# Optimization experiments

Measured on AMD Instinct MI355X. Metric: run time of the kernel, lower is better.

## Reference

```python
import jax, jax.numpy as jnp
import numpy as np

B, S, H, HEADS, STEP = 128, 256, 128, 8, 1


def setup_inputs() -> dict:
    key = jax.random.key(0)
    ks = jax.random.split(key, 20)
    rn = lambda k, shape: jax.random.normal(k, shape, dtype=jnp.float32) * 0.1
    return {
        "A": jax.random.uniform(ks[0], (B, S, 2 * S), dtype=jnp.float32),
        "hidden": jax.random.normal(ks[1], (B, S, H), dtype=jnp.float32),
        "mask": jnp.ones((B, S), dtype=jnp.int32),
        "w_ih": rn(ks[2], (3 * H, 2 * H)),
        "w_hh": rn(ks[3], (3 * H, H)),
        "b_ih": rn(ks[4], (3 * H,)),
        "b_hh": rn(ks[5], (3 * H,)),
        "b_iah": rn(ks[6], (H,)),
        "b_oah": rn(ks[7], (H,)),
        "W_ein": rn(ks[8], (H, H)), "b_ein": rn(ks[9], (H,)),
        "W_eout": rn(ks[10], (H, H)), "b_eout": rn(ks[11], (H,)),
        "W_q0": rn(ks[12], (H, H)), "b_q0": rn(ks[13], (H,)),
        "W_q1": rn(ks[14], (H, H)), "b_q1": rn(ks[15], (H,)),
        "W_q2": rn(ks[16], (H, H)), "b_q2": rn(ks[17], (H,)),
    }


def _forward(A, hidden, mask, w_ih, w_hh, b_ih, b_hh, b_iah, b_oah,
             W_ein, b_ein, W_eout, b_eout, W_q0, b_q0, W_q1, b_q1, W_q2, b_q2):
    b, s, h = hidden.shape
    dk = h // HEADS
    # ---- GNN: gated graph propagation (GRU cell over adjacency messages) ----
    for _ in range(STEP):
        msg_in = A[:, :, :s] @ (hidden @ W_ein.T + b_ein) + b_iah    # [B,S,H]
        msg_out = A[:, :, s:] @ (hidden @ W_eout.T + b_eout) + b_oah  # [B,S,H]
        inputs = jnp.concatenate([msg_in, msg_out], axis=2)           # [B,S,2H]
        gi = inputs @ w_ih.T + b_ih                                   # [B,S,3H]
        gh = hidden @ w_hh.T + b_hh                                   # [B,S,3H]
        i_r, i_i, i_n = jnp.split(gi, 3, axis=2)
        h_r, h_i, h_n = jnp.split(gh, 3, axis=2)
        resetgate = jax.nn.sigmoid(i_r + h_r)
        inputgate = jax.nn.sigmoid(i_i + h_i)
        newgate = jnp.tanh(i_n + resetgate * h_n)
        hidden = hidden - inputgate * (hidden - newgate)
    # ---- query: hidden state of the last valid item in each session ----
    last_idx = jnp.sum(mask, axis=1) - 1
    ht1 = hidden[jnp.arange(b), last_idx]                             # [B,H]
    # ---- LastAttenion: sigmoid score + double softmax readout ----
    q0 = (ht1 @ W_q0.T + b_q0).reshape(b, HEADS, dk)                  # [B,h,dk]
    q1 = (hidden @ W_q1.T + b_q1).reshape(b, s, HEADS, dk).transpose(0, 2, 1, 3)
    q2 = (hidden @ W_q2.T + b_q2).reshape(b, s, HEADS, dk).transpose(0, 2, 1, 3)
    # q0 is expanded over the query axis, so every score row is identical
    alpha = jax.nn.sigmoid(jnp.einsum('bhd,bhjd->bhj', q0, q1))        # [B,h,S]
    alpha = jnp.broadcast_to(alpha[:, :, None, :], (b, HEADS, s, s))   # [B,h,S,S]
    alpha = jax.nn.softmax(alpha, axis=-1)
    row_keep = (mask > 0)[:, None, :, None]                            # [B,1,S,1]
    alpha = jnp.where(row_keep, alpha, -jnp.inf)
    alpha = jax.nn.softmax(2.0 * alpha, axis=1)                        # over heads
    alpha = jnp.where(row_keep, alpha, 0.0)  # guard fully-masked rows (torch would NaN)
    x = jnp.einsum('bhij,bhjd->bhid', alpha, q2)                       # [B,h,S,dk]
    x = x.transpose(0, 2, 1, 3).reshape(b, s, h)                       # [B,S,H]
    a = jnp.sum(x * mask[:, :, None].astype(x.dtype), axis=1)          # [B,H]
    return a


def reference(A, hidden, mask, w_ih, w_hh, b_ih, b_hh, b_iah, b_oah,
              W_ein, b_ein, W_eout, b_eout, W_q0, b_q0, W_q1, b_q1, W_q2, b_q2):
    return _forward(A, hidden, mask, w_ih, w_hh, b_ih, b_hh, b_iah, b_oah,
                    W_ein, b_ein, W_eout, b_eout, W_q0, b_q0, W_q1, b_q1, W_q2, b_q2)
```

## Files before the change

### kernel.cpp

```cpp
#include <hip/hip_runtime.h>
#include <cstdint>
#include <cstddef>

#define BB   128
#define SS   256
#define HH   128
#define NH   8
#define DKK  16

typedef unsigned short u16;
typedef __attribute__((ext_vector_type(8))) short   sh8;
typedef __attribute__((ext_vector_type(4))) float   f32x4;

__device__ __forceinline__ float sigmoidf_(float x) { return 1.f / (1.f + expf(-x)); }

__device__ __forceinline__ u16 f2bf(float x) {
    union { float f; unsigned int u; } v; v.f = x;
    unsigned int r = (v.u + 0x7fffu + ((v.u >> 16) & 1u)) >> 16;
    return (u16)r;
}
__device__ __forceinline__ float bf2f(u16 u) {
    union { unsigned int u; float f; } v; v.u = ((unsigned int)u) << 16;
    return v.f;
}

#define BKk 32
#define PK  40

template<int XMODE, int OMODE>
__global__ __launch_bounds__(256) void gemm_mfma(
    const void* __restrict__ Xa, const void* __restrict__ Xc, int ldx, int ldx1, int ksplit,
    long long sXb, long long sXh,
    const u16* __restrict__ Bw, int ldb, long long sBb, long long sBh,
    const float* __restrict__ bias,
    void* __restrict__ Out, long long ldo, long long sOb, long long sOh,
    int K)
{
    __shared__ u16 As[128 * PK];
    __shared__ u16 Bs[128 * PK];

    const int t  = threadIdx.x;
    const int bm = blockIdx.x * 128;
    const int bn = blockIdx.y * 128;
    const long long zb = blockIdx.z >> 1, zh = blockIdx.z & 1;

    const u16* Bp = Bw + zb * sBb + zh * sBh;

    const int wave = t >> 6, lane = t & 63;
    const int wr = (wave >> 1) * 64, wc = (wave & 1) * 64;
    const int fm = lane & 15, fq = lane >> 4;

    f32x4 acc[4][4] = {};

    const int r0  = t >> 2, kk0 = (t & 3) * 8;
    const int r1  = t >> 3, kk1 = (t & 7) * 4;

    for (int k0 = 0; k0 < K; k0 += BKk) {
        if (XMODE == 1) {
            const float* Xf = (const float*)Xa + zb * sXb + zh * sXh;
            #pragma unroll
            for (int c = 0; c < 4; c++) {
                int r = r1 + 32 * c;
                float4 v = *(const float4*)(Xf + (long long)(bm + r) * ldx + k0 + kk1);
                ushort4 w = { f2bf(v.x), f2bf(v.y), f2bf(v.z), f2bf(v.w) };
                *(ushort4*)&As[r * PK + kk1] = w;
            }
        } else {
            #pragma unroll
            for (int c = 0; c < 2; c++) {
                int r = r0 + 64 * c;
                const u16* src;
                if (XMODE == 2 && k0 >= ksplit)
                    src = (const u16*)Xc + (long long)(bm + r) * ldx1 + (k0 - ksplit) + kk0;
                else
                    src = (const u16*)Xa + (long long)(bm + r) * ldx + k0 + kk0;
                uint4 v = *(const uint4*)src;
                *(uint4*)&As[r * PK + kk0] = v;
            }
        }
        #pragma unroll
        for (int c = 0; c < 2; c++) {
            int r = r0 + 64 * c;
            uint4 v = *(const uint4*)(Bp + (long long)(bn + r) * ldb + k0 + kk0);
            *(uint4*)&Bs[r * PK + kk0] = v;
        }
        __syncthreads();

        sh8 af[4], bfr[4];
        #pragma unroll
        for (int i = 0; i < 4; i++) af[i]  = *(const sh8*)&As[(wr + i * 16 + fm) * PK + fq * 8];
        #pragma unroll
        for (int j = 0; j < 4; j++) bfr[j] = *(const sh8*)&Bs[(wc + j * 16 + fm) * PK + fq * 8];
        #pragma unroll
        for (int i = 0; i < 4; i++)
            #pragma unroll
            for (int j = 0; j < 4; j++)
                acc[i][j] = __builtin_amdgcn_mfma_f32_16x16x32_bf16(af[i], bfr[j], acc[i][j], 0, 0, 0);
        __syncthreads();
    }

    #pragma unroll
    for (int j = 0; j < 4; j++) {
        const int col = bn + wc + j * 16 + fm;
        const float bj = bias ? bias[col] : 0.f;
        #pragma unroll
        for (int i = 0; i < 4; i++) {
            const int row0 = bm + wr + i * 16 + fq * 4;
            if (OMODE == 0) {
                float* O = (float*)Out + zb * sOb + zh * sOh;
                #pragma unroll
                for (int r = 0; r < 4; r++)
                    O[(long long)(row0 + r) * ldo + col] = acc[i][j][r] + bj;
            } else if (OMODE == 1) {
                u16* O = (u16*)Out + zb * sOb + zh * sOh;
                #pragma unroll
                for (int r = 0; r < 4; r++)
                    O[(long long)(row0 + r) * ldo + col] = f2bf(acc[i][j][r] + bj);
            } else {
                u16* O = (u16*)Out + zb * sOb + zh * sOh;
                ushort4 w = { f2bf(acc[i][j][0] + bj), f2bf(acc[i][j][1] + bj),
                              f2bf(acc[i][j][2] + bj), f2bf(acc[i][j][3] + bj) };
                *(ushort4*)&O[(long long)col * ldo + row0] = w;
            }
        }
    }
}

__global__ __launch_bounds__(256) void k_prepw(
    const float* __restrict__ w_ih, const float* __restrict__ w_hh,
    const float* __restrict__ b_ih, const float* __restrict__ b_hh,
    const float* __restrict__ b_iah, const float* __restrict__ b_oah,
    const float* __restrict__ W_ein, const float* __restrict__ b_ein,
    const float* __restrict__ W_eout, const float* __restrict__ b_eout,
    const float* __restrict__ W_q1, const float* __restrict__ b_q1,
    const float* __restrict__ W_q2, const float* __restrict__ b_q2,
    u16* __restrict__ W2bf, float* __restrict__ bias2,
    u16* __restrict__ Wcat, float* __restrict__ biascat,
    u16* __restrict__ Wq12, float* __restrict__ biasq12)
{
    int idx = blockIdx.x * 256 + threadIdx.x;
    if (idx < 512 * 384) {
        int n = idx / 384, kk = idx % 384;
        float v;
        if (n < 384) v = (kk < 256) ? w_ih[n * 256 + kk]
                                    : (n < 256 ? w_hh[n * 128 + kk - 256] : 0.f);
        else         v = (kk < 256) ? 0.f : w_hh[(n - 128) * 128 + kk - 256];
        W2bf[idx] = f2bf(v);
    }
    if (idx < 256 * 128) {
        int n = idx >> 7, k = idx & 127;
        Wcat[idx] = f2bf(n < 128 ? W_ein[n * 128 + k] : W_eout[(n - 128) * 128 + k]);
        Wq12[idx] = f2bf(n < 128 ? W_q1[n * 128 + k]  : W_q2[(n - 128) * 128 + k]);
    }
    if (idx < 512) {
        int n = idx;
        float s;
        if (n < 256)      s = b_ih[n] + b_hh[n];
        else if (n < 384) s = b_ih[n];
        else              s = b_hh[n - 128];
        if (n < 384) {
            for (int k = 0; k < 128; k++)
                s += w_ih[n * 256 + k] * b_iah[k] + w_ih[n * 256 + 128 + k] * b_oah[k];
        }
        bias2[n] = s;
    }
    if (idx < 256) {
        biascat[idx] = idx < 128 ? b_ein[idx] : b_eout[idx - 128];
        biasq12[idx] = idx < 128 ? b_q1[idx]  : b_q2[idx - 128];
    }
}

__global__ __launch_bounds__(256) void k_cast4(const float* __restrict__ in,
                                               u16* __restrict__ outp, int n4)
{
    int i = blockIdx.x * 256 + threadIdx.x;
    if (i < n4) {
        float4 v = ((const float4*)in)[i];
        ushort4 w = { f2bf(v.x), f2bf(v.y), f2bf(v.z), f2bf(v.w) };
        ((ushort4*)outp)[i] = w;
    }
}

__global__ void k_mask(const int* __restrict__ mask, int* __restrict__ lastidx,
                       int* __restrict__ nvalid)
{
    int b = threadIdx.x;
    int s = 0;
    for (int j = 0; j < SS; j++) s += mask[b * SS + j];
    nvalid[b] = s;
    lastidx[b] = (s - 1) & (SS - 1);
}

__global__ __launch_bounds__(256) void k_gates(const float* __restrict__ g4,
                                               const float* __restrict__ hidden,
                                               u16* __restrict__ hnew_bf)
{
    size_t idx = (size_t)blockIdx.x * 256 + threadIdx.x;
    int c = (int)(idx & 127);
    size_t row = idx >> 7;
    const float* g = g4 + row * 512;
    float gr  = g[c];
    float gi  = g[128 + c];
    float in_ = g[256 + c];
    float hn  = g[384 + c];
    float h = hidden[idx];
    float r  = sigmoidf_(gr);
    float ig = sigmoidf_(gi);
    float ng = tanhf(in_ + r * hn);
    hnew_bf[idx] = f2bf(h - ig * (h - ng));
}

__global__ void k_q0(const u16* __restrict__ hnew_bf, const int* __restrict__ lastidx,
                     const float* __restrict__ Wq0, const float* __restrict__ bq0,
                     float* __restrict__ q0buf)
{
    int b = blockIdx.x;
    int n = threadIdx.x;
    __shared__ float hs[HH];
    const u16* hrow = hnew_bf + ((size_t)b * SS + lastidx[b]) * HH;
    hs[n] = bf2f(hrow[n]);
    __syncthreads();
    float s = bq0[n];
    const float* w = Wq0 + (size_t)n * HH;
    #pragma unroll 8
    for (int k = 0; k < HH; k++) s += hs[k] * w[k];
    q0buf[(size_t)b * HH + n] = s;
}

__global__ __launch_bounds__(256) void k_scores(const float* __restrict__ q0buf,
                                                const float* __restrict__ q12,
                                                float* __restrict__ pbuf)
{
    int h = blockIdx.x;
    int b = blockIdx.y;
    int j = threadIdx.x;
    __shared__ float q0s[DKK];
    __shared__ float red[SS];
    if (j < DKK) q0s[j] = q0buf[(size_t)b * HH + h * DKK + j];
    __syncthreads();

    const float4* q1p = (const float4*)(q12 + ((size_t)b * SS + j) * 256 + h * DKK);
    float4 v0 = q1p[0], v1 = q1p[1], v2 = q1p[2], v3 = q1p[3];
    float s = 0.f;
    s += q0s[0] * v0.x + q0s[1] * v0.y + q0s[2] * v0.z + q0s[3] * v0.w;
    s += q0s[4] * v1.x + q0s[5] * v1.y + q0s[6] * v1.z + q0s[7] * v1.w;
    s += q0s[8] * v2.x + q0s[9] * v2.y + q0s[10] * v2.z + q0s[11] * v2.w;
    s += q0s[12] * v3.x + q0s[13] * v3.y + q0s[14] * v3.z + q0s[15] * v3.w;
    float a = sigmoidf_(s);

    red[j] = a;
    __syncthreads();
    for (int off = 128; off > 0; off >>= 1) {
        if (j < off) red[j] = fmaxf(red[j], red[j + off]);
        __syncthreads();
    }
    float m = red[0];
    __syncthreads();
    float e = expf(a - m);
    red[j] = e;
    __syncthreads();
    for (int off = 128; off > 0; off >>= 1) {
        if (j < off) red[j] += red[j + off];
        __syncthreads();
    }
    float denom = red[0];
    pbuf[((size_t)b * NH + h) * SS + j] = e / denom;
}

__global__ __launch_bounds__(128) void k_readout(const float* __restrict__ pbuf,
                                                 const float* __restrict__ q12,
                                                 const int* __restrict__ nvalid,
                                                 float* __restrict__ out)
{
    int b = blockIdx.x;
    int t = threadIdx.x;
    __shared__ float w_s[NH][SS];

    #pragma unroll
    for (int jj = 0; jj < 2; jj++) {
        int j = t + jj * 128;
        float e[NH];
        float den = 0.f;
        #pragma unroll
        for (int h = 0; h < NH; h++) {
            float p = pbuf[((size_t)b * NH + h) * SS + j];
            e[h] = expf(2.f * p);
            den += e[h];
        }
        float inv = 1.f / den;
        #pragma unroll
        for (int h = 0; h < NH; h++) w_s[h][j] = e[h] * inv;
    }
    __syncthreads();

    int h = t >> 4;
    float acc = 0.f;
    const float* q2b = q12 + (size_t)b * SS * 256 + 128 + t;
    for (int j = 0; j < SS; j++) acc += w_s[h][j] * q2b[(size_t)j * 256];
    out[(size_t)b * HH + t] = acc * (float)nvalid[b];
}

extern "C" void kernel_launch(void* const* d_in, const int* in_sizes, int n_in,
                              void* d_out, int out_size, void* d_ws, size_t ws_size,
                              hipStream_t stream)
{
    const float* A      = (const float*)d_in[0];
    const float* hidden = (const float*)d_in[1];
    const int*   mask   = (const int*)d_in[2];
    const float* w_ih   = (const float*)d_in[3];
    const float* w_hh   = (const float*)d_in[4];
    const float* b_ih   = (const float*)d_in[5];
    const float* b_hh   = (const float*)d_in[6];
    const float* b_iah  = (const float*)d_in[7];
    const float* b_oah  = (const float*)d_in[8];
    const float* W_ein  = (const float*)d_in[9];
    const float* b_ein  = (const float*)d_in[10];
    const float* W_eout = (const float*)d_in[11];
    const float* b_eout = (const float*)d_in[12];
    const float* W_q0   = (const float*)d_in[13];
    const float* b_q0   = (const float*)d_in[14];
    const float* W_q1   = (const float*)d_in[15];
    const float* b_q1   = (const float*)d_in[16];
    const float* W_q2   = (const float*)d_in[17];
    const float* b_q2   = (const float*)d_in[18];
    float* out = (float*)d_out;
    char* ws = (char*)d_ws;

    u16*   Et      = (u16*)(ws + 0);
    u16*   Mbuf    = (u16*)(ws + 16777216);
    float* q12     = (float*)(ws + 0);
    u16*   h_bf    = (u16*)(ws + 33554432);
    u16*   hnew_bf = (u16*)(ws + 41943040);
    u16*   W2bf    = (u16*)(ws + 50331648);
    u16*   Wcat    = (u16*)(ws + 50724864);
    u16*   Wq12    = (u16*)(ws + 50790400);
    float* bias2   = (float*)(ws + 50855936);
    float* biascat = (float*)(ws + 50857984);
    float* biasq12 = (float*)(ws + 50859008);
    float* q0buf   = (float*)(ws + 50860032);
    float* pbuf    = (float*)(ws + 50925568);
    int*   lastidx = (int*)(ws + 51974144);
    int*   nvalid  = (int*)(ws + 51974656);
    float* g4 = (float*)d_in[0];

    k_prepw<<<768, 256, 0, stream>>>(w_ih, w_hh, b_ih, b_hh, b_iah, b_oah,
                                     W_ein, b_ein, W_eout, b_eout,
                                     W_q1, b_q1, W_q2, b_q2,
                                     W2bf, bias2, Wcat, biascat, Wq12, biasq12);
    k_mask<<<1, 128, 0, stream>>>(mask, lastidx, nvalid);
    k_cast4<<<4096, 256, 0, stream>>>(hidden, h_bf, 1048576);

    gemm_mfma<0, 2><<<dim3(256, 2, 1), 256, 0, stream>>>(
        h_bf, nullptr, 128, 0, 0, 0, 0,
        Wcat, 128, 0, 0, biascat,
        Et, 32768, 0, 0, 128);

    gemm_mfma<1, 1><<<dim3(2, 1, 256), 256, 0, stream>>>(
        A, nullptr, 512, 0, 0, 131072LL, 256LL,
        Et, 32768, 256LL, 128LL * 32768LL, nullptr,
        Mbuf, 256, 65536LL, 128LL, 256);

    gemm_mfma<2, 0><<<dim3(256, 4, 1), 256, 0, stream>>>(
        Mbuf, h_bf, 256, 128, 256, 0, 0,
        W2bf, 384, 0, 0, bias2,
        g4, 512, 0, 0, 384);

    k_gates<<<16384, 256, 0, stream>>>(g4, hidden, hnew_bf);

    gemm_mfma<0, 0><<<dim3(256, 2, 1), 256, 0, stream>>>(
        hnew_bf, nullptr, 128, 0, 0, 0, 0,
        Wq12, 128, 0, 0, biasq12,
        q12, 256, 0, 0, 128);

    k_q0<<<BB, HH, 0, stream>>>(hnew_bf, lastidx, W_q0, b_q0, q0buf);
    k_scores<<<dim3(NH, BB), SS, 0, stream>>>(q0buf, q12, pbuf);
    k_readout<<<BB, HH, 0, stream>>>(pbuf, q12, nvalid, out);
}
```

Baseline: 258.8 us.

## Fuse GRU gates into GEMM epilogue, fold hidden cast, merge attention tail

Interleaves the GRU weight rows so each group of four output columns holds r/i/n_in/n_h for one channel. The gate math then runs in the GEMM epilogue through lane shuffles, which removes the fp32 g4 round-trip and the separate gates kernel. The hidden→bf16 cast is folded into the GEMM A-load path, q1/q2 are stored as bf16, and the mask/q0/scores/readout kernels are merged into one per-batch tail kernel. This cuts launches and memory traffic. In exchange, the epilogue uses scattered stores with a quarter of the lanes active, and q12 loses precision by going to bf16.

```diff
diff --git a/kernel.cpp b/kernel.cpp
--- a/kernel.cpp
+++ b/kernel.cpp
@@ -34,7 +34,7 @@
     const u16* __restrict__ Bw, int ldb, long long sBb, long long sBh,
     const float* __restrict__ bias,
     void* __restrict__ Out, long long ldo, long long sOb, long long sOh,
-    int K)
+    int K, const float* __restrict__ hid)
 {
     __shared__ u16 As[128 * PK];
     __shared__ u16 Bs[128 * PK];
@@ -56,12 +56,18 @@
     const int r1  = t >> 3, kk1 = (t & 7) * 4;
 
     for (int k0 = 0; k0 < K; k0 += BKk) {
-        if (XMODE == 1) {
-            const float* Xf = (const float*)Xa + zb * sXb + zh * sXh;
+        if (XMODE == 1 || (XMODE == 3 && k0 >= ksplit)) {
+            const float* Xf;
+            int kb, ld;
+            if (XMODE == 1) {
+                Xf = (const float*)Xa + zb * sXb + zh * sXh; kb = k0; ld = ldx;
+            } else {
+                Xf = (const float*)Xc; kb = k0 - ksplit; ld = ldx1;
+            }
             #pragma unroll
             for (int c = 0; c < 4; c++) {
                 int r = r1 + 32 * c;
-                float4 v = *(const float4*)(Xf + (long long)(bm + r) * ldx + k0 + kk1);
+                float4 v = *(const float4*)(Xf + (long long)(bm + r) * ld + kb + kk1);
                 ushort4 w = { f2bf(v.x), f2bf(v.y), f2bf(v.z), f2bf(v.w) };
                 *(ushort4*)&As[r * PK + kk1] = w;
             }
@@ -69,11 +75,7 @@
             #pragma unroll
             for (int c = 0; c < 2; c++) {
                 int r = r0 + 64 * c;
-                const u16* src;
-                if (XMODE == 2 && k0 >= ksplit)
-                    src = (const u16*)Xc + (long long)(bm + r) * ldx1 + (k0 - ksplit) + kk0;
-                else
-                    src = (const u16*)Xa + (long long)(bm + r) * ldx + k0 + kk0;
+                const u16* src = (const u16*)Xa + (long long)(bm + r) * ldx + k0 + kk0;
                 uint4 v = *(const uint4*)src;
                 *(uint4*)&As[r * PK + kk0] = v;
             }
@@ -106,21 +108,35 @@
         #pragma unroll
         for (int i = 0; i < 4; i++) {
             const int row0 = bm + wr + i * 16 + fq * 4;
-            if (OMODE == 0) {
-                float* O = (float*)Out + zb * sOb + zh * sOh;
-                #pragma unroll
-                for (int r = 0; r < 4; r++)
-                    O[(long long)(row0 + r) * ldo + col] = acc[i][j][r] + bj;
-            } else if (OMODE == 1) {
+            if (OMODE == 1) {
                 u16* O = (u16*)Out + zb * sOb + zh * sOh;
                 #pragma unroll
                 for (int r = 0; r < 4; r++)
                     O[(long long)(row0 + r) * ldo + col] = f2bf(acc[i][j][r] + bj);
-            } else {
+            } else if (OMODE == 2) {
                 u16* O = (u16*)Out + zb * sOb + zh * sOh;
                 ushort4 w = { f2bf(acc[i][j][0] + bj), f2bf(acc[i][j][1] + bj),
                               f2bf(acc[i][j][2] + bj), f2bf(acc[i][j][3] + bj) };
                 *(ushort4*)&O[(long long)col * ldo + row0] = w;
+            } else {
+                u16* O = (u16*)Out;
+                const bool act = (fm & 3) == 0;
+                const int ch = ((bn + wc + j * 16) >> 2) + (fm >> 2);
+                #pragma unroll
+                for (int r = 0; r < 4; r++) {
+                    float v  = acc[i][j][r] + bj;
+                    float a1 = __shfl_xor(v, 1);
+                    float a2 = __shfl_xor(v, 2);
+                    float a3 = __shfl_xor(a1, 2);
+                    if (act) {
+                        const int row = row0 + r;
+                        float h  = hid[(long long)row * HH + ch];
+                        float rg = sigmoidf_(v);
+                        float ig = sigmoidf_(a1);
+                        float ng = tanhf(a2 + rg * a3);
+                        O[(long long)row * ldo + ch] = f2bf(h - ig * (h - ng));
+                    }
+                }
             }
         }
     }
@@ -140,11 +156,13 @@
 {
     int idx = blockIdx.x * 256 + threadIdx.x;
     if (idx < 512 * 384) {
-        int n = idx / 384, kk = idx % 384;
+        int np = idx / 384, kk = idx % 384;
+        int c = np >> 2, g = np & 3;
         float v;
-        if (n < 384) v = (kk < 256) ? w_ih[n * 256 + kk]
-                                    : (n < 256 ? w_hh[n * 128 + kk - 256] : 0.f);
-        else         v = (kk < 256) ? 0.f : w_hh[(n - 128) * 128 + kk - 256];
+        if (g < 2)       v = (kk < 256) ? w_ih[(g * 128 + c) * 256 + kk]
+                                        : w_hh[(g * 128 + c) * 128 + kk - 256];
+        else if (g == 2) v = (kk < 256) ? w_ih[(256 + c) * 256 + kk] : 0.f;
+        else             v = (kk < 256) ? 0.f : w_hh[(256 + c) * 128 + kk - 256];
         W2bf[idx] = f2bf(v);
     }
     if (idx < 256 * 128) {
@@ -153,16 +171,17 @@
         Wq12[idx] = f2bf(n < 128 ? W_q1[n * 128 + k]  : W_q2[(n - 128) * 128 + k]);
     }
     if (idx < 512) {
-        int n = idx;
+        int np = idx, c = np >> 2, g = np & 3;
         float s;
-        if (n < 256)      s = b_ih[n] + b_hh[n];
-        else if (n < 384) s = b_ih[n];
-        else              s = b_hh[n - 128];
-        if (n < 384) {
+        if (g < 2)       s = b_ih[g * 128 + c] + b_hh[g * 128 + c];
+        else if (g == 2) s = b_ih[256 + c];
+        else             s = b_hh[256 + c];
+        if (g < 3) {
+            int n = (g < 2) ? g * 128 + c : 256 + c;
             for (int k = 0; k < 128; k++)
                 s += w_ih[n * 256 + k] * b_iah[k] + w_ih[n * 256 + 128 + k] * b_oah[k];
         }
-        bias2[n] = s;
+        bias2[np] = s;
     }
     if (idx < 256) {
         biascat[idx] = idx < 128 ? b_ein[idx] : b_eout[idx - 128];
@@ -170,134 +189,96 @@
     }
 }
 
-__global__ __launch_bounds__(256) void k_cast4(const float* __restrict__ in,
-                                               u16* __restrict__ outp, int n4)
+__global__ __launch_bounds__(256) void k_tail(
+    const u16* __restrict__ hnew_bf, const int* __restrict__ mask,
+    const u16* __restrict__ q12, const float* __restrict__ Wq0,
+    const float* __restrict__ bq0, float* __restrict__ out)
 {
-    int i = blockIdx.x * 256 + threadIdx.x;
-    if (i < n4) {
-        float4 v = ((const float4*)in)[i];
-        ushort4 w = { f2bf(v.x), f2bf(v.y), f2bf(v.z), f2bf(v.w) };
-        ((ushort4*)outp)[i] = w;
-    }
-}
-
-__global__ void k_mask(const int* __restrict__ mask, int* __restrict__ lastidx,
-                       int* __restrict__ nvalid)
-{
-    int b = threadIdx.x;
-    int s = 0;
-    for (int j = 0; j < SS; j++) s += mask[b * SS + j];
-    nvalid[b] = s;
-    lastidx[b] = (s - 1) & (SS - 1);
-}
-
-__global__ __launch_bounds__(256) void k_gates(const float* __restrict__ g4,
-                                               const float* __restrict__ hidden,
-                                               u16* __restrict__ hnew_bf)
-{
-    size_t idx = (size_t)blockIdx.x * 256 + threadIdx.x;
-    int c = (int)(idx & 127);
-    size_t row = idx >> 7;
-    const float* g = g4 + row * 512;
-    float gr  = g[c];
-    float gi  = g[128 + c];
-    float in_ = g[256 + c];
-    float hn  = g[384 + c];
-    float h = hidden[idx];
-    float r  = sigmoidf_(gr);
-    float ig = sigmoidf_(gi);
-    float ng = tanhf(in_ + r * hn);
-    hnew_bf[idx] = f2bf(h - ig * (h - ng));
-}
-
-__global__ void k_q0(const u16* __restrict__ hnew_bf, const int* __restrict__ lastidx,
-                     const float* __restrict__ Wq0, const float* __restrict__ bq0,
-                     float* __restrict__ q0buf)
-{
-    int b = blockIdx.x;
-    int n = threadIdx.x;
+    const int b = blockIdx.x, t = threadIdx.x;
+    __shared__ float red[256];
     __shared__ float hs[HH];
-    const u16* hrow = hnew_bf + ((size_t)b * SS + lastidx[b]) * HH;
-    hs[n] = bf2f(hrow[n]);
-    __syncthreads();
-    float s = bq0[n];
-    const float* w = Wq0 + (size_t)n * HH;
-    #pragma unroll 8
-    for (int k = 0; k < HH; k++) s += hs[k] * w[k];
-    q0buf[(size_t)b * HH + n] = s;
-}
-
-__global__ __launch_bounds__(256) void k_scores(const float* __restrict__ q0buf,
-                                                const float* __restrict__ q12,
-                                                float* __restrict__ pbuf)
-{
-    int h = blockIdx.x;
-    int b = blockIdx.y;
-    int j = threadIdx.x;
-    __shared__ float q0s[DKK];
-    __shared__ float red[SS];
-    if (j < DKK) q0s[j] = q0buf[(size_t)b * HH + h * DKK + j];
-    __syncthreads();
-
-    const float4* q1p = (const float4*)(q12 + ((size_t)b * SS + j) * 256 + h * DKK);
-    float4 v0 = q1p[0], v1 = q1p[1], v2 = q1p[2], v3 = q1p[3];
-    float s = 0.f;
-    s += q0s[0] * v0.x + q0s[1] * v0.y + q0s[2] * v0.z + q0s[3] * v0.w;
-    s += q0s[4] * v1.x + q0s[5] * v1.y + q0s[6] * v1.z + q0s[7] * v1.w;
-    s += q0s[8] * v2.x + q0s[9] * v2.y + q0s[10] * v2.z + q0s[11] * v2.w;
-    s += q0s[12] * v3.x + q0s[13] * v3.y + q0s[14] * v3.z + q0s[15] * v3.w;
-    float a = sigmoidf_(s);
-
-    red[j] = a;
+    __shared__ float q0s[HH];
+    __shared__ float p_s[NH][SS];
+    __shared__ float w_s[NH][SS];
+    __shared__ int s_nv;
+
+    red[t] = (float)mask[b * SS + t];
     __syncthreads();
     for (int off = 128; off > 0; off >>= 1) {
-        if (j < off) red[j] = fmaxf(red[j], red[j + off]);
+        if (t < off) red[t] += red[t + off];
         __syncthreads();
     }
-    float m = red[0];
-    __syncthreads();
-    float e = expf(a - m);
-    red[j] = e;
-    __syncthreads();
-    for (int off = 128; off > 0; off >>= 1) {
-        if (j < off) red[j] += red[j + off];
-        __syncthreads();
-    }
-    float denom = red[0];
-    pbuf[((size_t)b * NH + h) * SS + j] = e / denom;
-}
-
-__global__ __launch_bounds__(128) void k_readout(const float* __restrict__ pbuf,
-                                                 const float* __restrict__ q12,
-                                                 const int* __restrict__ nvalid,
-                                                 float* __restrict__ out)
-{
-    int b = blockIdx.x;
-    int t = threadIdx.x;
-    __shared__ float w_s[NH][SS];
-
-    #pragma unroll
-    for (int jj = 0; jj < 2; jj++) {
-        int j = t + jj * 128;
-        float e[NH];
-        float den = 0.f;
+    if (t == 0) s_nv = (int)red[0];
+    __syncthreads();
+    const int nv = s_nv;
+    const int last = (nv - 1) & (SS - 1);
+
+    if (t < HH) hs[t] = bf2f(hnew_bf[((size_t)b * SS + last) * HH + t]);
+    __syncthreads();
+
+    {
+        const int n = t & 127, kh = t >> 7;
+        const float* w = Wq0 + (size_t)n * HH + kh * 64;
+        float s = 0.f;
+        #pragma unroll 16
+        for (int k = 0; k < 64; k++) s += hs[kh * 64 + k] * w[k];
+        red[t] = s;
+    }
+    __syncthreads();
+    if (t < HH) q0s[t] = red[t] + red[t + 128] + bq0[t];
+    __syncthreads();
+
+    {
+        const u16* q1r = q12 + ((size_t)b * SS + t) * 256;
         #pragma unroll
         for (int h = 0; h < NH; h++) {
-            float p = pbuf[((size_t)b * NH + h) * SS + j];
-            e[h] = expf(2.f * p);
-            den += e[h];
-        }
-        float inv = 1.f / den;
-        #pragma unroll
-        for (int h = 0; h < NH; h++) w_s[h][j] = e[h] * inv;
-    }
-    __syncthreads();
-
-    int h = t >> 4;
-    float acc = 0.f;
-    const float* q2b = q12 + (size_t)b * SS * 256 + 128 + t;
-    for (int j = 0; j < SS; j++) acc += w_s[h][j] * q2b[(size_t)j * 256];
-    out[(size_t)b * HH + t] = acc * (float)nvalid[b];
+            float s = 0.f;
+            #pragma unroll
+            for (int d = 0; d < DKK; d++) s += q0s[h * DKK + d] * bf2f(q1r[h * DKK + d]);
+            p_s[h][t] = sigmoidf_(s);
+        }
+    }
+    __syncthreads();
+
+    {
+        const int h = t >> 5, l = t & 31;
+        float v[8], m = -1e30f;
+        #pragma unroll
+        for (int u = 0; u < 8; u++) { v[u] = p_s[h][l * 8 + u]; m = fmaxf(m, v[u]); }
+        #pragma unroll
+        for (int msk = 1; msk < 32; msk <<= 1) m = fmaxf(m, __shfl_xor(m, msk, 32));
+        float sum = 0.f;
+        #pragma unroll
+        for (int u = 0; u < 8; u++) { v[u] = expf(v[u] - m); sum += v[u]; }
+        #pragma unroll
+        for (int msk = 1; msk < 32; msk <<= 1) sum += __shfl_xor(sum, msk, 32);
+        const float inv = 1.f / sum;
+        #pragma unroll
+        for (int u = 0; u < 8; u++) p_s[h][l * 8 + u] = v[u] * inv;
+    }
+    __syncthreads();
+
+    {
+        float e[NH], den = 0.f;
+        #pragma unroll
+        for (int h = 0; h < NH; h++) { e[h] = expf(2.f * p_s[h][t]); den += e[h]; }
+        const float inv = 1.f / den;
+        #pragma unroll
+        for (int h = 0; h < NH; h++) w_s[h][t] = e[h] * inv;
+    }
+    __syncthreads();
+
+    {
+        const int col = t & 127, jh = t >> 7;
+        const int h = col >> 4;
+        const u16* q2b = q12 + (size_t)b * SS * 256 + 128 + col;
+        float acc = 0.f;
+        for (int j = jh * 128; j < jh * 128 + 128; j++)
+            acc += w_s[h][j] * bf2f(q2b[(size_t)j * 256]);
+        red[t] = acc;
+    }
+    __syncthreads();
+    if (t < HH) out[(size_t)b * HH + t] = (red[t] + red[t + 128]) * (float)nv;
 }
 
 extern "C" void kernel_launch(void* const* d_in, const int* in_sizes, int n_in,
@@ -328,51 +309,39 @@
 
     u16*   Et      = (u16*)(ws + 0);
     u16*   Mbuf    = (u16*)(ws + 16777216);
-    float* q12     = (float*)(ws + 0);
-    u16*   h_bf    = (u16*)(ws + 33554432);
-    u16*   hnew_bf = (u16*)(ws + 41943040);
-    u16*   W2bf    = (u16*)(ws + 50331648);
-    u16*   Wcat    = (u16*)(ws + 50724864);
-    u16*   Wq12    = (u16*)(ws + 50790400);
-    float* bias2   = (float*)(ws + 50855936);
-    float* biascat = (float*)(ws + 50857984);
-    float* biasq12 = (float*)(ws + 50859008);
-    float* q0buf   = (float*)(ws + 50860032);
-    float* pbuf    = (float*)(ws + 50925568);
-    int*   lastidx = (int*)(ws + 51974144);
-    int*   nvalid  = (int*)(ws + 51974656);
-    float* g4 = (float*)d_in[0];
+    u16*   q12bf   = (u16*)(ws + 0);
+    u16*   hnew_bf = (u16*)(ws + 33554432);
+    u16*   W2bf    = (u16*)(ws + 41943040);
+    u16*   Wcat    = (u16*)(ws + 42336256);
+    u16*   Wq12    = (u16*)(ws + 42401792);
+    float* bias2   = (float*)(ws + 42467328);
+    float* biascat = (float*)(ws + 42469376);
+    float* biasq12 = (float*)(ws + 42470400);
 
     k_prepw<<<768, 256, 0, stream>>>(w_ih, w_hh, b_ih, b_hh, b_iah, b_oah,
                                      W_ein, b_ein, W_eout, b_eout,
                                      W_q1, b_q1, W_q2, b_q2,
                                      W2bf, bias2, Wcat, biascat, Wq12, biasq12);
-    k_mask<<<1, 128, 0, stream>>>(mask, lastidx, nvalid);
-    k_cast4<<<4096, 256, 0, stream>>>(hidden, h_bf, 1048576);
-
-    gemm_mfma<0, 2><<<dim3(256, 2, 1), 256, 0, stream>>>(
-        h_bf, nullptr, 128, 0, 0, 0, 0,
-        Wcat, 128, 0, 0, biascat,
-        Et, 32768, 0, 0, 128);
+
+    gemm_mfma<1, 2><<<dim3(256, 2, 1), 256, 0, stream>>>(
+        hidden, nullptr, HH, 0, 0, 0, 0,
+        Wcat, HH, 0, 0, biascat,
+        Et, 32768, 0, 0, HH, nullptr);
 
     gemm_mfma<1, 1><<<dim3(2, 1, 256), 256, 0, stream>>>(
         A, nullptr, 512, 0, 0, 131072LL, 256LL,
         Et, 32768, 256LL, 128LL * 32768LL, nullptr,
-        Mbuf, 256, 65536LL, 128LL, 256);
-
-    gemm_mfma<2, 0><<<dim3(256, 4, 1), 256, 0, stream>>>(
-        Mbuf, h_bf, 256, 128, 256, 0, 0,
+        Mbuf, 256, 65536LL, 128LL, SS, nullptr);
+
+    gemm_mfma<3, 3><<<dim3(256, 4, 1), 256, 0, stream>>>(
+        Mbuf, hidden, 256, HH, 256, 0, 0,
         W2bf, 384, 0, 0, bias2,
-        g4, 512, 0, 0, 384);
-
-    k_gates<<<16384, 256, 0, stream>>>(g4, hidden, hnew_bf);
-
-    gemm_mfma<0, 0><<<dim3(256, 2, 1), 256, 0, stream>>>(
-        hnew_bf, nullptr, 128, 0, 0, 0, 0,
-        Wq12, 128, 0, 0, biasq12,
-        q12, 256, 0, 0, 128);
-
-    k_q0<<<BB, HH, 0, stream>>>(hnew_bf, lastidx, W_q0, b_q0, q0buf);
-    k_scores<<<dim3(NH, BB), SS, 0, stream>>>(q0buf, q12, pbuf);
-    k_readout<<<BB, HH, 0, stream>>>(pbuf, q12, nvalid, out);
-}
+        hnew_bf, HH, 0, 0, 384, hidden);
+
+    gemm_mfma<0, 1><<<dim3(256, 2, 1), 256, 0, stream>>>(
+        hnew_bf, nullptr, HH, 0, 0, 0, 0,
+        Wq12, HH, 0, 0, biasq12,
+        q12bf, 256, 0, 0, HH, nullptr);
+
+    k_tail<<<BB, 256, 0, stream>>>(hnew_bf, mask, q12bf, W_q0, b_q0, out);
+}
```

Result: slower. 291.7 us (+12.7%).
